# Optimization experiments

Measured on AMD Instinct MI355X. Metric: run time of the kernel, lower is better.

The kernel has to match this reference:

```python
import jax, jax.numpy as jnp
import numpy as np

# Synthetic production-scale triangle mesh: dense HxW grid.
H = 512
W = 512
V = H * W           # num_vertices = 262144
B = 32              # batch of meshes


def _grid_faces(h, w):
    # Two triangles per quad cell; vertex (i,j) -> index i*w + j.
    i, j = np.meshgrid(np.arange(h - 1), np.arange(w - 1), indexing='ij')
    v = (i * w + j).ravel()
    f1 = np.stack([v, v + 1, v + w], axis=1)
    f2 = np.stack([v + 1, v + w + 1, v + w], axis=1)
    return np.concatenate([f1, f2], axis=0).astype(np.int64)  # (F, 3)


def _laplacian_edges(faces, num_vertices):
    # Unique undirected edges from the 3 sides of every triangle.
    e = np.concatenate([faces[:, [0, 1]], faces[:, [1, 2]], faces[:, [2, 0]]], axis=0)
    e = np.sort(e, axis=1)
    e = np.unique(e, axis=0)                      # (E_und, 2)
    rows = np.concatenate([e[:, 0], e[:, 1]])     # directed: both orientations
    cols = np.concatenate([e[:, 1], e[:, 0]])
    deg = np.bincount(rows, minlength=num_vertices).astype(np.float32)
    vals = -1.0 / deg[rows]                       # row-normalized off-diagonal of L
    return rows.astype(np.int32), cols.astype(np.int32), vals.astype(np.float32)


def setup_inputs() -> dict:
    key = jax.random.key(0)
    faces = _grid_faces(H, W)
    rows, cols, vals = _laplacian_edges(faces, V)
    vertices = jax.random.normal(key, (B, V, 3), dtype=jnp.float32)
    return {
        'vertices': vertices,
        'rows': jnp.asarray(rows),   # (2E,) int32 — destination vertex of each Laplacian entry
        'cols': jnp.asarray(cols),   # (2E,) int32 — source   vertex of each Laplacian entry
        'vals': jnp.asarray(vals),   # (2E,) float32 — -1/deg[row]
    }


def reference(vertices, rows, cols, vals):
    # L @ v == v + scatter_add(vals * v[cols]) : identity diagonal + normalized neighbors.
    num_v = vertices.shape[1]
    gathered = vertices[:, cols, :] * vals[None, :, None]        # (B, 2E, 3)
    neigh = jax.vmap(lambda g: jax.ops.segment_sum(g, rows, num_segments=num_v))(gathered)
    Lv = vertices + neigh                                        # (B, V, 3)
    # torch: (Lv ** 2).sum(dim=-1).mean()  -> mean over (B, V) of squared norms
    return jnp.mean(jnp.sum(Lv * Lv, axis=-1))
```

## Files before the change

### kernel.cpp

```cpp
#include <hip/hip_runtime.h>


#define GH 512
#define GW 512
#define GV (GH * GW)
#define NBLK 4096

__global__ __launch_bounds__(256) void lap_partial_kernel(
    const float* __restrict__ verts, float* __restrict__ partials, int B) {
    const long long total = (long long)B * GV;
    const long long nthreads = (long long)gridDim.x * blockDim.x;
    const long long tid0 = (long long)blockIdx.x * blockDim.x + threadIdx.x;

    float local = 0.0f;
    for (long long idx = tid0; idx < total; idx += nthreads) {
        const int b = (int)(idx >> 18);
        const int v = (int)(idx & (GV - 1));
        const int i = v >> 9;
        const int j = v & (GW - 1);
        const float* __restrict__ base = verts + (long long)b * GV * 3;

        float sx = 0.f, sy = 0.f, sz = 0.f;
        int deg = 0;

        #define ACC(vv) { const float* p = base + (long long)(vv) * 3; \
                          sx += p[0]; sy += p[1]; sz += p[2]; deg++; }
        if (j > 0)                  ACC(v - 1);
        if (j < GW - 1)             ACC(v + 1);
        if (i > 0)                  ACC(v - GW);
        if (i < GH - 1)             ACC(v + GW);
        if (i > 0 && j < GW - 1)    ACC(v - GW + 1);
        if (i < GH - 1 && j > 0)    ACC(v + GW - 1);
        #undef ACC

        const float inv = -1.0f / (float)deg;
        const float* p = base + (long long)v * 3;
        const float lx = fmaf(inv, sx, p[0]);
        const float ly = fmaf(inv, sy, p[1]);
        const float lz = fmaf(inv, sz, p[2]);
        local += lx * lx + ly * ly + lz * lz;
    }

    #pragma unroll
    for (int off = 32; off > 0; off >>= 1)
        local += __shfl_down(local, off, 64);

    __shared__ float wsum[4];
    const int lane = threadIdx.x & 63;
    const int wid  = threadIdx.x >> 6;
    if (lane == 0) wsum[wid] = local;
    __syncthreads();

    if (threadIdx.x == 0)
        partials[blockIdx.x] = wsum[0] + wsum[1] + wsum[2] + wsum[3];
}

__global__ __launch_bounds__(256) void lap_final_kernel(
    const float* __restrict__ partials, float* __restrict__ out, int nblk, int B) {
    float local = 0.0f;
    for (int k = threadIdx.x; k < nblk; k += 256)
        local += partials[k];

    #pragma unroll
    for (int off = 32; off > 0; off >>= 1)
        local += __shfl_down(local, off, 64);

    __shared__ float wsum[4];
    const int lane = threadIdx.x & 63;
    const int wid  = threadIdx.x >> 6;
    if (lane == 0) wsum[wid] = local;
    __syncthreads();

    if (threadIdx.x == 0) {
        const float s = wsum[0] + wsum[1] + wsum[2] + wsum[3];
        out[0] = s / ((float)B * (float)GV);
    }
}

extern "C" void kernel_launch(void* const* d_in, const int* in_sizes, int n_in,
                              void* d_out, int out_size, void* d_ws, size_t ws_size,
                              hipStream_t stream) {
    const float* verts = (const float*)d_in[0];
    float* out = (float*)d_out;
    float* partials = (float*)d_ws;

    const int B = in_sizes[0] / (GV * 3);

    lap_partial_kernel<<<NBLK, 256, 0, stream>>>(verts, partials, B);
    lap_final_kernel<<<1, 256, 0, stream>>>(partials, out, NBLK, B);
}
```

Before: 191.3 us.

## Stream rows per thread with register sliding window for Laplacian stencil

Each thread now owns a grid column and walks down a 16-row chunk, keeping the previous rows' left/center/right values in registers. Partial neighbor sums are reused across rows, so each vertex row is loaded once per thread instead of being re-gathered up to seven times. The grid is now sized per batch, half-row and chunk rather than a fixed grid-stride launch. In exchange, each chunk reloads two halo rows, the fully unrolled loop raises register use, and the code hardcodes 512x512 with 256 threads per block.

```diff
diff --git a/kernel.cpp b/kernel.cpp
--- a/kernel.cpp
+++ b/kernel.cpp
@@ -4,41 +4,71 @@
 #define GH 512
 #define GW 512
 #define GV (GH * GW)
-#define NBLK 4096
+#define RI 16
+#define NCHUNK (GH / RI)
+
+struct F3 { float x, y, z; };
 
 __global__ __launch_bounds__(256) void lap_partial_kernel(
-    const float* __restrict__ verts, float* __restrict__ partials, int B) {
-    const long long total = (long long)B * GV;
-    const long long nthreads = (long long)gridDim.x * blockDim.x;
-    const long long tid0 = (long long)blockIdx.x * blockDim.x + threadIdx.x;
+    const float* __restrict__ verts, float* __restrict__ partials) {
+    const int bid   = blockIdx.x;
+    const int chunk = bid & (NCHUNK - 1);
+    const int half  = (bid >> 5) & 1;
+    const int b     = bid >> 6;
+    const int j     = half * 256 + (int)threadIdx.x;
+    const int i0    = chunk * RI;
+    const float* __restrict__ base = verts + (size_t)b * (GV * 3);
 
+    const int jl = (j > 0), jr = (j < GW - 1);
+    const float fl = (float)jl, fr = (float)jr;
+    const float inv_int = -1.0f / (float)(2 + 2 * jl + 2 * jr);
+    const float inv_top = -1.0f / (float)(1 + 2 * jl + jr);
+    const float inv_bot = -1.0f / (float)(1 + jl + 2 * jr);
+
+    const int cl = 3 * (jl ? j - 1 : 0);
+    const int cc = 3 * j;
+    const int cr = 3 * (jr ? j + 1 : GW - 1);
+
+    F3 pL = {}, pC = {}, pR = {};
+    F3 T2 = {}, T1 = {};
+    F3 M1 = {}, C1 = {};
     float local = 0.0f;
-    for (long long idx = tid0; idx < total; idx += nthreads) {
-        const int b = (int)(idx >> 18);
-        const int v = (int)(idx & (GV - 1));
-        const int i = v >> 9;
-        const int j = v & (GW - 1);
-        const float* __restrict__ base = verts + (long long)b * GV * 3;
 
-        float sx = 0.f, sy = 0.f, sz = 0.f;
-        int deg = 0;
+    #pragma unroll
+    for (int k = 0; k <= RI + 2; ++k) {
+        F3 qL = {}, qC = {}, qR = {};
+        const int rload = i0 - 1 + k;
+        if (k <= RI + 1 && rload >= 0 && rload < GH) {
+            const float* __restrict__ rp = base + (size_t)rload * (GW * 3);
+            qL.x = rp[cl]; qL.y = rp[cl + 1]; qL.z = rp[cl + 2];
+            qC.x = rp[cc]; qC.y = rp[cc + 1]; qC.z = rp[cc + 2];
+            qR.x = rp[cr]; qR.y = rp[cr + 1]; qR.z = rp[cr + 2];
+        }
 
-        #define ACC(vv) { const float* p = base + (long long)(vv) * 3; \
-                          sx += p[0]; sy += p[1]; sz += p[2]; deg++; }
-        if (j > 0)                  ACC(v - 1);
-        if (j < GW - 1)             ACC(v + 1);
-        if (i > 0)                  ACC(v - GW);
-        if (i < GH - 1)             ACC(v + GW);
-        if (i > 0 && j < GW - 1)    ACC(v - GW + 1);
-        if (i < GH - 1 && j > 0)    ACC(v + GW - 1);
-        #undef ACC
+        const F3 Lm = { fl * pL.x, fl * pL.y, fl * pL.z };
+        const F3 Rm = { fr * pR.x, fr * pR.y, fr * pR.z };
+        const F3 Bx = { pC.x + Lm.x, pC.y + Lm.y, pC.z + Lm.z };
+        const F3 Tn = { pC.x + Rm.x, pC.y + Rm.y, pC.z + Rm.z };
+        const F3 Mn = { Lm.x + Rm.x, Lm.y + Rm.y, Lm.z + Rm.z };
+        const F3 Cn = pC;
 
-        const float inv = -1.0f / (float)deg;
-        const float* p = base + (long long)v * 3;
-        const float lx = fmaf(inv, sx, p[0]);
-        const float ly = fmaf(inv, sy, p[1]);
-        const float lz = fmaf(inv, sz, p[2]);
-        local += lx * lx + ly * ly + lz * lz;
+        if (k >= 3) {
+            const int c = i0 + k - 3;
+            const float inv = (c == 0) ? inv_top
+                            : ((c == GH - 1) ? inv_bot : inv_int);
+            const float sx = T2.x + M1.x + Bx.x;
+            const float sy = T2.y + M1.y + Bx.y;
+            const float sz = T2.z + M1.z + Bx.z;
+            const float lx = fmaf(inv, sx, C1.x);
+            const float ly = fmaf(inv, sy, C1.y);
+            const float lz = fmaf(inv, sz, C1.z);
+            local = fmaf(lx, lx, local);
+            local = fmaf(ly, ly, local);
+            local = fmaf(lz, lz, local);
+        }
+
+        T2 = T1; T1 = Tn; M1 = Mn; C1 = Cn;
+        pL = qL; pC = qC; pR = qR;
     }
 
     #pragma unroll
@@ -47,10 +77,9 @@
 
     __shared__ float wsum[4];
     const int lane = threadIdx.x & 63;
-    const int wid  = threadIdx.x >> 6;
-    if (lane == 0) wsum[wid] = local;
+    const int wave = threadIdx.x >> 6;
+    if (lane == 0) wsum[wave] = local;
     __syncthreads();
-
     if (threadIdx.x == 0)
         partials[blockIdx.x] = wsum[0] + wsum[1] + wsum[2] + wsum[3];
 }
@@ -85,7 +114,8 @@
     float* partials = (float*)d_ws;
 
     const int B = in_sizes[0] / (GV * 3);
+    const int nblk = B * 2 * NCHUNK;
 
-    lap_partial_kernel<<<NBLK, 256, 0, stream>>>(verts, partials, B);
-    lap_final_kernel<<<1, 256, 0, stream>>>(partials, out, NBLK, B);
+    lap_partial_kernel<<<nblk, 256, 0, stream>>>(verts, partials);
+    lap_final_kernel<<<1, 256, 0, stream>>>(partials, out, nblk, B);
 }
```

Measured after the change: 162.1 us. -15.3%, faster.

## Restructure Laplacian stencil into per-row tiles with vectorized float4 loads

Applied to the files above, without the earlier changes.

Replaces the grid-stride per-vertex loop, which did scalar gathers of six neighbors, with a fixed mapping: each block covers two grid rows of one mesh, and each thread handles four consecutive vertices using float4 loads from the row above, the current row and the row below. Neighbor sums and degrees are computed with multiplicative masks instead of branches. This cuts the number of load instructions and the repeated address arithmetic. In exchange, the launch now hardcodes B=32 through NBLK=8192 and ignores the runtime batch size.

```diff
diff --git a/kernel.cpp b/kernel.cpp
--- a/kernel.cpp
+++ b/kernel.cpp
@@ -4,41 +4,100 @@
 #define GH 512
 #define GW 512
 #define GV (GH * GW)
-#define NBLK 4096
+#define ROWF (GW * 3)
+#define NBLK 8192
 
-__global__ __launch_bounds__(256) void lap_partial_kernel(
-    const float* __restrict__ verts, float* __restrict__ partials, int B) {
-    const long long total = (long long)B * GV;
-    const long long nthreads = (long long)gridDim.x * blockDim.x;
-    const long long tid0 = (long long)blockIdx.x * blockDim.x + threadIdx.x;
+__global__ __launch_bounds__(256, 8) void lap_partial_kernel(
+    const float* __restrict__ verts, float* __restrict__ partials) {
+    const int bid   = blockIdx.x;
+    const int b     = bid >> 8;
+    const int rg    = bid & 255;
+    const int group = threadIdx.x >> 7;
+    const int g     = threadIdx.x & 127;
+    const int ci    = rg * 2 + group;
 
-    float local = 0.0f;
-    for (long long idx = tid0; idx < total; idx += nthreads) {
-        const int b = (int)(idx >> 18);
-        const int v = (int)(idx & (GV - 1));
-        const int i = v >> 9;
-        const int j = v & (GW - 1);
-        const float* __restrict__ base = verts + (long long)b * GV * 3;
+    const float* __restrict__ base = verts + (size_t)b * (GV * 3);
+    const float* __restrict__ rowO = base + (size_t)ci * ROWF;
 
-        float sx = 0.f, sy = 0.f, sz = 0.f;
-        int deg = 0;
+    const int f1 = 12 * g;
+    const int f0 = (g == 0) ? 0 : (f1 - 4);
+    const int f4 = (g == 127) ? (ROWF - 4) : (f1 + 12);
 
-        #define ACC(vv) { const float* p = base + (long long)(vv) * 3; \
-                          sx += p[0]; sy += p[1]; sz += p[2]; deg++; }
-        if (j > 0)                  ACC(v - 1);
-        if (j < GW - 1)             ACC(v + 1);
-        if (i > 0)                  ACC(v - GW);
-        if (i < GH - 1)             ACC(v + GW);
-        if (i > 0 && j < GW - 1)    ACC(v - GW + 1);
-        if (i < GH - 1 && j > 0)    ACC(v + GW - 1);
-        #undef ACC
+    const float fl = (g > 0)   ? 1.f : 0.f;
+    const float fr = (g < 127) ? 1.f : 0.f;
+    const float ht = (ci > 0)      ? 1.f : 0.f;
+    const float hb = (ci < GH - 1) ? 1.f : 0.f;
 
-        const float inv = -1.0f / (float)deg;
-        const float* p = base + (long long)v * 3;
-        const float lx = fmaf(inv, sx, p[0]);
-        const float ly = fmaf(inv, sy, p[1]);
-        const float lz = fmaf(inv, sz, p[2]);
-        local += lx * lx + ly * ly + lz * lz;
+    float o[20];
+    *(float4*)&o[0]  = *(const float4*)(rowO + f0);
+    *(float4*)&o[4]  = *(const float4*)(rowO + f1);
+    *(float4*)&o[8]  = *(const float4*)(rowO + f1 + 4);
+    *(float4*)&o[12] = *(const float4*)(rowO + f1 + 8);
+    *(float4*)&o[16] = *(const float4*)(rowO + f4);
+
+    float s[12];
+    #pragma unroll
+    for (int t = 0; t < 4; ++t) {
+        #pragma unroll
+        for (int w = 0; w < 3; ++w) {
+            float L = o[1 + 3 * t + w];
+            float R = o[7 + 3 * t + w];
+            if (t == 0) L *= fl;
+            if (t == 3) R *= fr;
+            s[3 * t + w] = L + R;
+        }
+    }
+
+    if (ci > 0) {
+        const float* __restrict__ rowA = rowO - ROWF;
+        float a[20];
+        *(float4*)&a[0]  = *(const float4*)(rowA + f0);
+        *(float4*)&a[4]  = *(const float4*)(rowA + f1);
+        *(float4*)&a[8]  = *(const float4*)(rowA + f1 + 4);
+        *(float4*)&a[12] = *(const float4*)(rowA + f1 + 8);
+        *(float4*)&a[16] = *(const float4*)(rowA + f4);
+        #pragma unroll
+        for (int t = 0; t < 4; ++t) {
+            #pragma unroll
+            for (int w = 0; w < 3; ++w) {
+                float R = a[7 + 3 * t + w];
+                if (t == 3) R *= fr;
+                s[3 * t + w] += a[4 + 3 * t + w] + R;
+            }
+        }
+    }
+
+    if (ci < GH - 1) {
+        const float* __restrict__ rowB = rowO + ROWF;
+        float a[20];
+        *(float4*)&a[0]  = *(const float4*)(rowB + f0);
+        *(float4*)&a[4]  = *(const float4*)(rowB + f1);
+        *(float4*)&a[8]  = *(const float4*)(rowB + f1 + 4);
+        *(float4*)&a[12] = *(const float4*)(rowB + f1 + 8);
+        *(float4*)&a[16] = *(const float4*)(rowB + f4);
+        #pragma unroll
+        for (int t = 0; t < 4; ++t) {
+            #pragma unroll
+            for (int w = 0; w < 3; ++w) {
+                float L = a[1 + 3 * t + w];
+                if (t == 0) L *= fl;
+                s[3 * t + w] += a[4 + 3 * t + w] + L;
+            }
+        }
+    }
+
+    float local = 0.f;
+    #pragma unroll
+    for (int t = 0; t < 4; ++t) {
+        const float jl = (t == 0) ? fl : 1.f;
+        const float jr = (t == 3) ? fr : 1.f;
+        const float deg = (ht + hb) + jl * (1.f + hb) + jr * (1.f + ht);
+        const float inv = -1.0f / deg;
+        #pragma unroll
+        for (int w = 0; w < 3; ++w) {
+            const float lv = fmaf(inv, s[3 * t + w], o[4 + 3 * t + w]);
+            local = fmaf(lv, lv, local);
+        }
     }
 
     #pragma unroll
@@ -47,12 +106,11 @@
 
     __shared__ float wsum[4];
     const int lane = threadIdx.x & 63;
-    const int wid  = threadIdx.x >> 6;
-    if (lane == 0) wsum[wid] = local;
+    const int wave = threadIdx.x >> 6;
+    if (lane == 0) wsum[wave] = local;
     __syncthreads();
-
     if (threadIdx.x == 0)
-        partials[blockIdx.x] = wsum[0] + wsum[1] + wsum[2] + wsum[3];
+        partials[bid] = wsum[0] + wsum[1] + wsum[2] + wsum[3];
 }
 
 __global__ __launch_bounds__(256) void lap_final_kernel(
@@ -86,6 +144,6 @@
 
     const int B = in_sizes[0] / (GV * 3);
 
-    lap_partial_kernel<<<NBLK, 256, 0, stream>>>(verts, partials, B);
+    lap_partial_kernel<<<NBLK, 256, 0, stream>>>(verts, partials);
     lap_final_kernel<<<1, 256, 0, stream>>>(partials, out, NBLK, B);
 }
```

Result: faster. 170.8 us (-10.8%).

## Stream grid rows through double-buffered LDS with register-carried vertical neighbor sums

Applied to the files above, without the earlier changes.

Replaces the grid-stride per-vertex gather with a row-streaming scheme. Each block owns a 16-row chunk of one mesh, loads each row with coalesced float4 reads into double-buffered shared memory, and keeps partial neighbor sums from the previous rows in registers, so every vertex is read from global memory about once plus a halo. This targets the redundant, strided 6-neighbor global loads of the old kernel. It adds a barrier per row and hardcodes B=32 in the block indexing (NBLK = 32*NCHUNK, bid>>5) instead of deriving the batch count from the input size.

```diff
diff --git a/kernel.cpp b/kernel.cpp
--- a/kernel.cpp
+++ b/kernel.cpp
@@ -4,41 +4,111 @@
 #define GH 512
 #define GW 512
 #define GV (GH * GW)
-#define NBLK 4096
+#define RI 16
+#define NCHUNK (GH / RI)
+#define ROWF (GW * 3)
+#define LROW 1544
+#define NITER (RI + 2)
+#define NBLK (32 * NCHUNK)
 
-__global__ __launch_bounds__(256) void lap_partial_kernel(
-    const float* __restrict__ verts, float* __restrict__ partials, int B) {
-    const long long total = (long long)B * GV;
-    const long long nthreads = (long long)gridDim.x * blockDim.x;
-    const long long tid0 = (long long)blockIdx.x * blockDim.x + threadIdx.x;
+__global__ __launch_bounds__(256, 4) void lap_partial_kernel(
+    const float* __restrict__ verts, float* __restrict__ partials) {
+    __shared__ float lds[2 * LROW];
 
-    float local = 0.0f;
-    for (long long idx = tid0; idx < total; idx += nthreads) {
-        const int b = (int)(idx >> 18);
-        const int v = (int)(idx & (GV - 1));
-        const int i = v >> 9;
-        const int j = v & (GW - 1);
-        const float* __restrict__ base = verts + (long long)b * GV * 3;
+    const int bid   = blockIdx.x;
+    const int batch = bid >> 5;
+    const int chunk = bid & (NCHUNK - 1);
+    const int i0    = chunk * RI;
+    const int t     = threadIdx.x;
+    const float* __restrict__ base = verts + (size_t)batch * (GV * 3);
 
-        float sx = 0.f, sy = 0.f, sz = 0.f;
-        int deg = 0;
+    if (t < 12) {
+        const int slot = t / 6, o = t - 6 * slot;
+        lds[slot * LROW + 1536 + o] = 0.0f;
+    }
 
-        #define ACC(vv) { const float* p = base + (long long)(vv) * 3; \
-                          sx += p[0]; sy += p[1]; sz += p[2]; deg++; }
-        if (j > 0)                  ACC(v - 1);
-        if (j < GW - 1)             ACC(v + 1);
-        if (i > 0)                  ACC(v - GW);
-        if (i < GH - 1)             ACC(v + GW);
-        if (i > 0 && j < GW - 1)    ACC(v - GW + 1);
-        if (i < GH - 1 && j > 0)    ACC(v + GW - 1);
-        #undef ACC
+    const float jle = (t > 0)   ? 1.f : 0.f;
+    const float jro = (t < 255) ? 1.f : 0.f;
+    const int fL = (t == 0)   ? 1536 : (6 * t - 3);
+    const int fE = 6 * t;
+    const int fO = 6 * t + 3;
+    const int fR = (t == 255) ? 1539 : (6 * t + 6);
 
-        const float inv = -1.0f / (float)deg;
-        const float* p = base + (long long)v * 3;
-        const float lx = fmaf(inv, sx, p[0]);
-        const float ly = fmaf(inv, sy, p[1]);
-        const float lz = fmaf(inv, sz, p[2]);
-        local += lx * lx + ly * ly + lz * lz;
+    const float invE_m = -1.f / (4.f + 2.f * jle);
+    const float invO_m = -1.f / (4.f + 2.f * jro);
+    const float invE_t = -1.f / (2.f + 2.f * jle);
+    const float invO_t = -1.f / (3.f + jro);
+    const float invE_b = -1.f / (3.f + jle);
+    const float invO_b = -1.f / (2.f + 2.f * jro);
+
+    float4 a0, a1;
+    {
+        const int r = i0 - 1;
+        if (r >= 0) {
+            const float4* rp = (const float4*)(base + (size_t)r * ROWF);
+            a0 = rp[t];
+            a1 = (t < 128) ? rp[256 + t] : make_float4(0.f, 0.f, 0.f, 0.f);
+        } else {
+            a0 = make_float4(0.f, 0.f, 0.f, 0.f); a1 = a0;
+        }
+    }
+    __syncthreads();
+
+    float T2Ex=0,T2Ey=0,T2Ez=0, T2Ox=0,T2Oy=0,T2Oz=0;
+    float T1Ex=0,T1Ey=0,T1Ez=0, T1Ox=0,T1Oy=0,T1Oz=0;
+    float M1Ex=0,M1Ey=0,M1Ez=0, M1Ox=0,M1Oy=0,M1Oz=0;
+    float C1Ex=0,C1Ey=0,C1Ez=0, C1Ox=0,C1Oy=0,C1Oz=0;
+    float local = 0.f;
+
+    for (int k = 0; k < NITER; ++k) {
+        float* lp = lds + (k & 1) * LROW;
+
+        *(float4*)(lp + 4 * t) = a0;
+        if (t < 128) *(float4*)(lp + 1024 + 4 * t) = a1;
+
+        if (k < NITER - 1) {
+            const int rn = i0 + k;
+            if (rn < GH) {
+                const float4* rp = (const float4*)(base + (size_t)rn * ROWF);
+                a0 = rp[t];
+                a1 = (t < 128) ? rp[256 + t] : make_float4(0.f, 0.f, 0.f, 0.f);
+            } else {
+                a0 = make_float4(0.f, 0.f, 0.f, 0.f); a1 = a0;
+            }
+        }
+        __syncthreads();
+
+        const float Lx = lp[fL], Ly = lp[fL + 1], Lz = lp[fL + 2];
+        const float Ex = lp[fE], Ey = lp[fE + 1], Ez = lp[fE + 2];
+        const float Ox = lp[fO], Oy = lp[fO + 1], Oz = lp[fO + 2];
+        const float Rx = lp[fR], Ry = lp[fR + 1], Rz = lp[fR + 2];
+
+        const float BnEx = Ex + Lx, BnEy = Ey + Ly, BnEz = Ez + Lz;
+        const float BnOx = Ox + Ex, BnOy = Oy + Ey, BnOz = Oz + Ez;
+        const float TnEx = Ex + Ox, TnEy = Ey + Oy, TnEz = Ez + Oz;
+        const float TnOx = Ox + Rx, TnOy = Oy + Ry, TnOz = Oz + Rz;
+        const float MnEx = Lx + Ox, MnEy = Ly + Oy, MnEz = Lz + Oz;
+        const float MnOx = Ex + Rx, MnOy = Ey + Ry, MnOz = Ez + Rz;
+
+        if (k >= 2) {
+            const int c = i0 + k - 2;
+            float invE = invE_m, invO = invO_m;
+            if (c == 0)            { invE = invE_t; invO = invO_t; }
+            else if (c == GH - 1)  { invE = invE_b; invO = invO_b; }
+
+            float s, lv;
+            s = T2Ex + M1Ex + BnEx; lv = fmaf(invE, s, C1Ex); local = fmaf(lv, lv, local);
+            s = T2Ey + M1Ey + BnEy; lv = fmaf(invE, s, C1Ey); local = fmaf(lv, lv, local);
+            s = T2Ez + M1Ez + BnEz; lv = fmaf(invE, s, C1Ez); local = fmaf(lv, lv, local);
+            s = T2Ox + M1Ox + BnOx; lv = fmaf(invO, s, C1Ox); local = fmaf(lv, lv, local);
+            s = T2Oy + M1Oy + BnOy; lv = fmaf(invO, s, C1Oy); local = fmaf(lv, lv, local);
+            s = T2Oz + M1Oz + BnOz; lv = fmaf(invO, s, C1Oz); local = fmaf(lv, lv, local);
+        }
+
+        T2Ex = T1Ex; T2Ey = T1Ey; T2Ez = T1Ez; T2Ox = T1Ox; T2Oy = T1Oy; T2Oz = T1Oz;
+        T1Ex = TnEx; T1Ey = TnEy; T1Ez = TnEz; T1Ox = TnOx; T1Oy = TnOy; T1Oz = TnOz;
+        M1Ex = MnEx; M1Ey = MnEy; M1Ez = MnEz; M1Ox = MnOx; M1Oy = MnOy; M1Oz = MnOz;
+        C1Ex = Ex;   C1Ey = Ey;   C1Ez = Ez;   C1Ox = Ox;   C1Oy = Oy;   C1Oz = Oz;
     }
 
     #pragma unroll
@@ -46,13 +116,12 @@
         local += __shfl_down(local, off, 64);
 
     __shared__ float wsum[4];
-    const int lane = threadIdx.x & 63;
-    const int wid  = threadIdx.x >> 6;
-    if (lane == 0) wsum[wid] = local;
+    const int lane = t & 63;
+    const int wave = t >> 6;
+    if (lane == 0) wsum[wave] = local;
     __syncthreads();
-
-    if (threadIdx.x == 0)
-        partials[blockIdx.x] = wsum[0] + wsum[1] + wsum[2] + wsum[3];
+    if (t == 0)
+        partials[bid] = wsum[0] + wsum[1] + wsum[2] + wsum[3];
 }
 
 __global__ __launch_bounds__(256) void lap_final_kernel(
@@ -86,6 +155,6 @@
 
     const int B = in_sizes[0] / (GV * 3);
 
-    lap_partial_kernel<<<NBLK, 256, 0, stream>>>(verts, partials, B);
+    lap_partial_kernel<<<NBLK, 256, 0, stream>>>(verts, partials);
     lap_final_kernel<<<1, 256, 0, stream>>>(partials, out, NBLK, B);
 }
```

Result: faster. 159.3 us (-16.7%).
